# Performance work log

Measured on AMD Instinct MI355X. Metric: run time of the kernel, lower is better.

The kernel has to match this reference:

```python
import jax, jax.numpy as jnp
import numpy as np

B = 64        # batch
L = 256       # latent_dim
H = 1024      # hidden
D = 1024      # mask dim
BAND = 16     # half-bandwidth of sparsity mask
M = 2 * BAND + 1  # max nnz per row (=33)


def _banded_mask_idx():
    """Build a banded (D,D) 0/1 mask and per-row column indices (D,M), -1 padded."""
    r = np.arange(D)
    mask = (np.abs(r[:, None] - r[None, :]) <= BAND).astype(np.float32)
    idx = np.full((D, M), -1, dtype=np.int32)
    for i in range(D):
        cols = np.nonzero(mask[i])[0]
        idx[i, :len(cols)] = cols
    return mask, idx


def setup_inputs() -> dict:
    key = jax.random.key(0)
    kz, k1, kb1, k2, kb2 = jax.random.split(key, 5)
    mask_np, idx_np = _banded_mask_idx()
    return {
        "z": jax.random.normal(kz, (B, L), dtype=jnp.float32),
        "mask": jnp.asarray(mask_np),
        "W1": jax.random.normal(k1, (L, H), dtype=jnp.float32) * 0.05,
        "b1": jax.random.normal(kb1, (H,), dtype=jnp.float32) * 0.05,
        "W2": jax.random.normal(k2, (H, D * M), dtype=jnp.float32) * 0.02,
        "b2": jax.random.normal(kb2, (D * M,), dtype=jnp.float32) * 0.02,
        "idx": jnp.asarray(idx_np),
    }


def reference(z, mask, W1, b1, W2, b2, idx):
    b = z.shape[0]
    # 2-layer MLP with exact (erf) GELU, as in nn.GELU()
    h = jax.nn.gelu(z @ W1 + b1, approximate=False)
    v = (h @ W2 + b2).reshape(b, D, M)          # (B, D, M)
    # scatter predicted values onto the mask support (unique targets -> add == set)
    valid = idx >= 0                             # (D, M)
    jc = jnp.where(valid, idx, 0)                # clamp -1 padding to col 0
    rows = jnp.broadcast_to(jnp.arange(D)[:, None], (D, M))
    vals = jnp.where(valid, v, jnp.zeros((), v.dtype))
    k = jnp.zeros((b, D, D), dtype=z.dtype).at[:, rows, jc].add(vals)
    # symmetrize, add identity, re-apply mask
    k = 0.5 * (k + jnp.swapaxes(k, -1, -2))
    k = k + jnp.eye(D, dtype=z.dtype)
    return k * mask[None, :, :]
```

## Files before the change

kernel.cpp:

```cpp
#include <hip/hip_runtime.h>
#include <math.h>

#define BATCH 64
#define LDIM  256
#define HDIM  1024
#define DDIM  1024
#define BAND  16
#define MNZ   33
#define NN    (DDIM*MNZ)
#define RTILE 64
#define LSTR  34

typedef float  v4f    __attribute__((ext_vector_type(4)));
typedef float  f32x4  __attribute__((ext_vector_type(4)));
typedef short  bf16x8 __attribute__((ext_vector_type(8)));
typedef unsigned short u16x8 __attribute__((ext_vector_type(8)));

static __device__ __forceinline__ unsigned short f2bf(float x) {
    union { float f; unsigned int u; } a; a.f = x;
    unsigned int r = a.u + 0x7fffu + ((a.u >> 16) & 1u);
    return (unsigned short)(r >> 16);
}

#define GLDS16(g, l)                                                         \
    __builtin_amdgcn_global_load_lds(                                        \
        (const __attribute__((address_space(1))) void*)(g),                  \
        (__attribute__((address_space(3))) void*)(l), 16, 0, 0)

__global__ __launch_bounds__(256) void k1_h(const float* __restrict__ z,
                                            const float* __restrict__ W1,
                                            const float* __restrict__ b1,
                                            unsigned short* __restrict__ hb) {
    __shared__ float zs[2][LDIM];
    const int t = threadIdx.x;
    const int b0 = blockIdx.x * 2;
    zs[0][t] = z[b0 * LDIM + t];
    zs[1][t] = z[(b0 + 1) * LDIM + t];
    __syncthreads();

    const int gid = blockIdx.x * 256 + t;
    const int b  = gid >> 7;
    const int j8 = gid & 127;
    const int j0 = j8 * 8;
    const float* __restrict__ zr = zs[t >> 7];

    float a[8];
#pragma unroll
    for (int c = 0; c < 8; ++c) a[c] = b1[j0 + c];
#pragma unroll 4
    for (int l = 0; l < LDIM; ++l) {
        const v4f w0 = *(const v4f*)&W1[(size_t)l * HDIM + j0];
        const v4f w1 = *(const v4f*)&W1[(size_t)l * HDIM + j0 + 4];
        const float zv = zr[l];
#pragma unroll
        for (int c = 0; c < 4; ++c) { a[c] = fmaf(zv, w0[c], a[c]); a[4 + c] = fmaf(zv, w1[c], a[4 + c]); }
    }
    u16x8 pk;
#pragma unroll
    for (int c = 0; c < 8; ++c) {
        const float g = 0.5f * a[c] * (1.0f + erff(a[c] * 0.70710678118654752f));
        pk[c] = f2bf(g);
    }
    const int s  = j8 >> 2;
    const int kq = j8 & 3;
    const int mt = b >> 4;
    const int nl = b & 15;
    ((u16x8*)hb)[(s * 4 + mt) * 64 + kq * 16 + nl] = pk;
}

__global__ __launch_bounds__(256) void k2_v(const float* __restrict__ W2,
                                            const float* __restrict__ b2,
                                            const unsigned short* __restrict__ hb,
                                            float* __restrict__ v) {
    __shared__ __align__(16) float          bt[4][32 * 64];
    __shared__ __align__(16) unsigned short at[4][4 * 512];
    const int tid  = threadIdx.x;
    const int lane = tid & 63;
    const int w    = __builtin_amdgcn_readfirstlane(tid >> 6);
    const int c0   = blockIdx.x * 64;
    const int kq   = lane >> 4;
    const int nl   = lane & 15;

    const int cg = (lane & 15) ^ (((w >> 1) & 1) << 2);
    const float* __restrict__ gB =
        W2 + (size_t)(4 * w + (lane >> 4)) * NN + c0 + cg * 4;
    const u16x8* __restrict__ gA = (const u16x8*)hb + w * 64 + lane;

    f32x4 acc[4];
#pragma unroll
    for (int mt = 0; mt < 4; ++mt) acc[mt] = (f32x4){0.f, 0.f, 0.f, 0.f};

    auto stage = [&](int slot, int s) {
        GLDS16(gB + (size_t)(s * 32) * NN,      &bt[slot][(4 * w) * 64]);
        GLDS16(gB + (size_t)(s * 32 + 16) * NN, &bt[slot][(16 + 4 * w) * 64]);
        GLDS16(gA + (size_t)s * 256,            &at[slot][w * 512]);
    };
    const int rcol = (w * 16 + nl) ^ ((kq & 1) << 4);
    auto compute = [&](int slot) {
        bf16x8 af[4];
#pragma unroll
        for (int mt = 0; mt < 4; ++mt)
            af[mt] = *(const bf16x8*)&at[slot][mt * 512 + lane * 8];
        float wv[8];
#pragma unroll
        for (int j = 0; j < 8; ++j)
            wv[j] = bt[slot][(kq * 8 + j) * 64 + rcol];
        bf16x8 bfr;
#pragma unroll
        for (int j = 0; j < 8; ++j) bfr[j] = (short)f2bf(wv[j]);
#pragma unroll
        for (int mt = 0; mt < 4; ++mt)
            acc[mt] = __builtin_amdgcn_mfma_f32_16x16x32_bf16(
                af[mt], bfr, acc[mt], 0, 0, 0);
    };

    stage(0, 0); stage(1, 1); stage(2, 2);

#pragma unroll 1
    for (int s = 0; s <= 28; ++s) {
        asm volatile("s_waitcnt vmcnt(6)" ::: "memory");
        __builtin_amdgcn_s_barrier();
        compute(s & 3);
        stage((s + 3) & 3, s + 3);
    }
    asm volatile("s_waitcnt vmcnt(6)" ::: "memory");
    __builtin_amdgcn_s_barrier();
    compute(29 & 3);
    asm volatile("s_waitcnt vmcnt(3)" ::: "memory");
    __builtin_amdgcn_s_barrier();
    compute(30 & 3);
    asm volatile("s_waitcnt vmcnt(0)" ::: "memory");
    __builtin_amdgcn_s_barrier();
    compute(31 & 3);

    const int col = c0 + w * 16 + nl;
    const float bias = b2[col];
    float* __restrict__ vo = v + col;
#pragma unroll
    for (int mt = 0; mt < 4; ++mt)
#pragma unroll
        for (int r = 0; r < 4; ++r)
            vo[(size_t)(mt * 16 + kq * 4 + r) * NN] = acc[mt][r] + bias;
}

__global__ __launch_bounds__(256) void k3_out(const float* __restrict__ v,
                                              float* __restrict__ out) {
    const int tid  = threadIdx.x;
    const int tile = blockIdx.x & (DDIM / RTILE - 1);
    const int b    = blockIdx.x / (DDIM / RTILE);
    const int i0 = tile * RTILE;
    const int js = (i0 >= BAND) ? (i0 - BAND) : 0;
    const int je = (i0 + RTILE + BAND <= DDIM) ? (i0 + RTILE + BAND) : DDIM;
    const int nelem = (je - js) * MNZ;

    __shared__ float ls[(RTILE + 2 * BAND) * LSTR];

    const float* __restrict__ vb = v + (size_t)b * NN + (size_t)js * MNZ;
    for (int idx = tid; idx < nelem; idx += 256) {
        const int r = idx / MNZ;
        const int m = idx - r * MNZ;
        ls[r * LSTR + m] = vb[idx];
    }
    __syncthreads();

    const int j0 = tid * 4;
#pragma unroll 2
    for (int r = 0; r < RTILE; ++r) {
        const int i = i0 + r;
        v4f res = (v4f){0.f, 0.f, 0.f, 0.f};
        if (j0 + 3 >= i - BAND && j0 <= i + BAND) {
            const int lo_i = (i > BAND) ? (i - BAND) : 0;
#pragma unroll
            for (int c = 0; c < 4; ++c) {
                const int j = j0 + c;
                const int d = j - i;
                float x = 0.0f;
                if (d >= -BAND && d <= BAND) {
                    const int lo_j = (j > BAND) ? (j - BAND) : 0;
                    x = 0.5f * (ls[(i - js) * LSTR + (j - lo_i)] +
                                ls[(j - js) * LSTR + (i - lo_j)]);
                    if (d == 0) x += 1.0f;
                }
                res[c] = x;
            }
        }
        v4f* dst = ((v4f*)out) + ((size_t)b * DDIM + i) * (DDIM / 4) + tid;
        __builtin_nontemporal_store(res, dst);
    }
}

extern "C" void kernel_launch(void* const* d_in, const int* in_sizes, int n_in,
                              void* d_out, int out_size, void* d_ws, size_t ws_size,
                              hipStream_t stream) {
    const float* z  = (const float*)d_in[0];
    const float* W1 = (const float*)d_in[2];
    const float* b1 = (const float*)d_in[3];
    const float* W2 = (const float*)d_in[4];
    const float* b2 = (const float*)d_in[5];

    unsigned short* hb = (unsigned short*)d_ws;
    float* v = (float*)((char*)d_ws + (size_t)BATCH * HDIM * sizeof(unsigned short));
    float* out = (float*)d_out;

    k1_h  <<<dim3(BATCH / 2), 256, 0, stream>>>(z, W1, b1, hb);
    k2_v  <<<dim3(NN / 64), 256, 0, stream>>>(W2, b2, hb, v);
    k3_out<<<dim3(BATCH * (DDIM / RTILE)), 256, 0, stream>>>(v, out);
}
```

Before: 433.2 us.

## Widen W2 GEMM tile to 256 columns per block with 4 n-tiles per wave

The second-layer GEMM kernel now processes 256 output columns per block instead of 64. Each wave computes a 4x4 grid of MFMA tiles, reusing the loaded activation fragments across four column tiles. Each wave issues eight W2 row loads per stage, and the wait counts are adjusted to match. This cuts the block count to 132 and raises LDS use to about 144KB, so only one block fits per CU and fewer than the 256 CUs get work, which risks lower memory-level parallelism when streaming W2.

```diff
diff --git a/kernel.cpp b/kernel.cpp
--- a/kernel.cpp
+++ b/kernel.cpp
@@ -72,75 +72,87 @@
                                             const float* __restrict__ b2,
                                             const unsigned short* __restrict__ hb,
                                             float* __restrict__ v) {
-    __shared__ __align__(16) float          bt[4][32 * 64];
-    __shared__ __align__(16) unsigned short at[4][4 * 512];
+    __shared__ __align__(16) float          bt[4][32 * 256];
+    __shared__ __align__(16) unsigned short at4[4][4 * 512];
     const int tid  = threadIdx.x;
     const int lane = tid & 63;
     const int w    = __builtin_amdgcn_readfirstlane(tid >> 6);
-    const int c0   = blockIdx.x * 64;
+    const int c0   = blockIdx.x * 256;
     const int kq   = lane >> 4;
     const int nl   = lane & 15;
 
-    const int cg = (lane & 15) ^ (((w >> 1) & 1) << 2);
-    const float* __restrict__ gB =
-        W2 + (size_t)(4 * w + (lane >> 4)) * NN + c0 + cg * 4;
+    const int scol = 4 * (lane ^ ((w & 1) << 2));
+    const float* __restrict__ gB = W2 + (size_t)(w * 8) * NN + c0 + scol;
     const u16x8* __restrict__ gA = (const u16x8*)hb + w * 64 + lane;
 
-    f32x4 acc[4];
-#pragma unroll
-    for (int mt = 0; mt < 4; ++mt) acc[mt] = (f32x4){0.f, 0.f, 0.f, 0.f};
+    f32x4 acc[4][4];
+#pragma unroll
+    for (int mt = 0; mt < 4; ++mt)
+#pragma unroll
+        for (int nt = 0; nt < 4; ++nt)
+            acc[mt][nt] = (f32x4){0.f, 0.f, 0.f, 0.f};
 
     auto stage = [&](int slot, int s) {
-        GLDS16(gB + (size_t)(s * 32) * NN,      &bt[slot][(4 * w) * 64]);
-        GLDS16(gB + (size_t)(s * 32 + 16) * NN, &bt[slot][(16 + 4 * w) * 64]);
-        GLDS16(gA + (size_t)s * 256,            &at[slot][w * 512]);
+#pragma unroll
+        for (int i = 0; i < 8; ++i)
+            GLDS16(gB + (size_t)(s * 32 + i) * NN, &bt[slot][(w * 8 + i) * 256]);
+        GLDS16(gA + (size_t)s * 256, &at4[slot][w * 512]);
     };
-    const int rcol = (w * 16 + nl) ^ ((kq & 1) << 4);
     auto compute = [&](int slot) {
         bf16x8 af[4];
 #pragma unroll
         for (int mt = 0; mt < 4; ++mt)
-            af[mt] = *(const bf16x8*)&at[slot][mt * 512 + lane * 8];
-        float wv[8];
-#pragma unroll
-        for (int j = 0; j < 8; ++j)
-            wv[j] = bt[slot][(kq * 8 + j) * 64 + rcol];
-        bf16x8 bfr;
-#pragma unroll
-        for (int j = 0; j < 8; ++j) bfr[j] = (short)f2bf(wv[j]);
+            af[mt] = *(const bf16x8*)&at4[slot][mt * 512 + lane * 8];
+        bf16x8 bfr[4];
+#pragma unroll
+        for (int nt = 0; nt < 4; ++nt) {
+            const int rc = (w * 64 + nt * 16 + nl) ^ ((kq & 1) << 4);
+            float wv[8];
+#pragma unroll
+            for (int j = 0; j < 8; ++j)
+                wv[j] = bt[slot][(kq * 8 + j) * 256 + rc];
+#pragma unroll
+            for (int j = 0; j < 8; ++j) bfr[nt][j] = (short)f2bf(wv[j]);
+        }
 #pragma unroll
         for (int mt = 0; mt < 4; ++mt)
-            acc[mt] = __builtin_amdgcn_mfma_f32_16x16x32_bf16(
-                af[mt], bfr, acc[mt], 0, 0, 0);
+#pragma unroll
+            for (int nt = 0; nt < 4; ++nt)
+                acc[mt][nt] = __builtin_amdgcn_mfma_f32_16x16x32_bf16(
+                    af[mt], bfr[nt], acc[mt][nt], 0, 0, 0);
     };
 
     stage(0, 0); stage(1, 1); stage(2, 2);
 
 #pragma unroll 1
     for (int s = 0; s <= 28; ++s) {
-        asm volatile("s_waitcnt vmcnt(6)" ::: "memory");
+        asm volatile("s_waitcnt vmcnt(18)" ::: "memory");
         __builtin_amdgcn_s_barrier();
         compute(s & 3);
         stage((s + 3) & 3, s + 3);
     }
-    asm volatile("s_waitcnt vmcnt(6)" ::: "memory");
+    asm volatile("s_waitcnt vmcnt(18)" ::: "memory");
     __builtin_amdgcn_s_barrier();
     compute(29 & 3);
-    asm volatile("s_waitcnt vmcnt(3)" ::: "memory");
+    asm volatile("s_waitcnt vmcnt(9)" ::: "memory");
     __builtin_amdgcn_s_barrier();
     compute(30 & 3);
     asm volatile("s_waitcnt vmcnt(0)" ::: "memory");
     __builtin_amdgcn_s_barrier();
     compute(31 & 3);
 
-    const int col = c0 + w * 16 + nl;
-    const float bias = b2[col];
-    float* __restrict__ vo = v + col;
-#pragma unroll
-    for (int mt = 0; mt < 4; ++mt)
-#pragma unroll
-        for (int r = 0; r < 4; ++r)
-            vo[(size_t)(mt * 16 + kq * 4 + r) * NN] = acc[mt][r] + bias;
+    const int colb = c0 + w * 64;
+#pragma unroll
+    for (int nt = 0; nt < 4; ++nt) {
+        const int col = colb + nt * 16 + nl;
+        const float bias = b2[col];
+        float* __restrict__ vo = v + col;
+#pragma unroll
+        for (int mt = 0; mt < 4; ++mt)
+#pragma unroll
+            for (int r = 0; r < 4; ++r)
+                vo[(size_t)(mt * 16 + kq * 4 + r) * NN] = acc[mt][nt][r] + bias;
+    }
 }
 
 __global__ __launch_bounds__(256) void k3_out(const float* __restrict__ v,
@@ -203,6 +215,6 @@
     float* out = (float*)d_out;
 
     k1_h  <<<dim3(BATCH / 2), 256, 0, stream>>>(z, W1, b1, hb);
-    k2_v  <<<dim3(NN / 64), 256, 0, stream>>>(W2, b2, hb, v);
+    k2_v  <<<dim3(NN / 256), 256, 0, stream>>>(W2, b2, hb, v);
     k3_out<<<dim3(BATCH * (DDIM / RTILE)), 256, 0, stream>>>(v, out);
 }
```

After: 426.7 us. About the same (-1.5%).
